# Optimization experiments

Measured on AMD Instinct MI355X. Metric: run time of the kernel, lower is better.

## Reference

```python
import jax, jax.numpy as jnp
import numpy as np

N_NODES = 100000
N_EDGES = 3200000
C, H, F = 512, 256, 64


def spmm(edge_row, edge_col, edge_val, Z):
    # (A @ Z)[i] = sum over edges e with row[e]==i of val[e] * Z[col[e]]
    msgs = edge_val[:, None] * Z[edge_col]  # [E, d]
    return jax.ops.segment_sum(msgs, edge_row, num_segments=N_NODES)


def setup_inputs() -> dict:
    key = jax.random.key(0)
    k1, k2, k3, k4, k5, k6, k7 = jax.random.split(key, 7)
    X = jax.random.normal(k1, (N_NODES, C), dtype=jnp.float32)
    edge_row = jax.random.randint(k2, (N_EDGES,), 0, N_NODES, dtype=jnp.int32)
    edge_col = jax.random.randint(k3, (N_EDGES,), 0, N_NODES, dtype=jnp.int32)
    edge_val = jax.random.uniform(k4, (N_EDGES,), dtype=jnp.float32)
    W0 = jax.random.normal(k5, (C, H), dtype=jnp.float32) * (C ** -0.5)
    Wh1 = jax.random.normal(k6, (H, H), dtype=jnp.float32) * (H ** -0.5)
    W1 = jax.random.normal(k7, (H, F), dtype=jnp.float32) * (H ** -0.5)
    return {"X": X, "edge_row": edge_row, "edge_col": edge_col,
            "edge_val": edge_val, "W0": W0, "Wh1": Wh1, "W1": W1}


def reference(X, edge_row, edge_col, edge_val, W0, Wh1, W1):
    # layer 0: relu(A @ (X W0))   (dropout=0 -> identity)
    Z = jax.nn.relu(spmm(edge_row, edge_col, edge_val, X @ W0))
    # hidden layers (num_layers - 2 = 1)
    Z = jax.nn.relu(spmm(edge_row, edge_col, edge_val, Z @ Wh1))
    # output layer: softmax(A @ (Z W1), axis=-1)
    Z = jax.nn.softmax(spmm(edge_row, edge_col, edge_val, Z @ W1), axis=-1)
    return Z
```

## Files before the change

kernel.cpp:

```cpp
#include <hip/hip_runtime.h>
#include <cstdint>
#include <cstddef>


#define SCAN_B 1024

typedef __attribute__((ext_vector_type(8))) short short8_t;
typedef __attribute__((ext_vector_type(4))) short short4_t;
typedef __attribute__((ext_vector_type(4))) float f32x4;

__device__ __forceinline__ short bf16_hi(float x) {
    union { float f; unsigned u; } c; c.f = x;
    return (short)(c.u >> 16);
}
__device__ __forceinline__ float bf16_f32(short h) {
    union { float f; unsigned u; } c; c.u = ((unsigned)(unsigned short)h) << 16;
    return c.f;
}

__device__ __forceinline__ void gload_lds16(const void* g, void* l) {
    __builtin_amdgcn_global_load_lds(
        (const __attribute__((address_space(1))) void*)g,
        (__attribute__((address_space(3))) void*)l, 16, 0, 0);
}


__global__ void count_rows_k(const int* __restrict__ row, int* __restrict__ deg, int E) {
    int e = blockIdx.x * blockDim.x + threadIdx.x;
    if (e < E) atomicAdd(&deg[row[e]], 1);
}

__global__ __launch_bounds__(SCAN_B) void scan1_k(const int* __restrict__ deg,
                                                  int* __restrict__ part,
                                                  int* __restrict__ bsum, int n) {
    __shared__ int buf[SCAN_B];
    int tid = threadIdx.x;
    int i = blockIdx.x * SCAN_B + tid;
    int v = (i < n) ? ((deg[i] + 3) & ~3) : 0;
    buf[tid] = v;
    __syncthreads();
    for (int off = 1; off < SCAN_B; off <<= 1) {
        int y = (tid >= off) ? buf[tid - off] : 0;
        __syncthreads();
        buf[tid] += y;
        __syncthreads();
    }
    if (i < n) part[i] = buf[tid] - v;
    if (tid == SCAN_B - 1) bsum[blockIdx.x] = buf[tid];
}

__global__ __launch_bounds__(128) void scan2_k(int* __restrict__ bsum, int nb) {
    __shared__ int buf[128];
    int tid = threadIdx.x;
    int v = (tid < nb) ? bsum[tid] : 0;
    buf[tid] = v;
    __syncthreads();
    for (int off = 1; off < 128; off <<= 1) {
        int y = (tid >= off) ? buf[tid - off] : 0;
        __syncthreads();
        buf[tid] += y;
        __syncthreads();
    }
    if (tid < nb) bsum[tid] = buf[tid] - v;
    if (tid == nb - 1) bsum[nb] = buf[tid];
}

__global__ __launch_bounds__(SCAN_B) void scan3_k(int* __restrict__ rowptr,
                                                  const int* __restrict__ bsum,
                                                  int* __restrict__ cursor, int n, int nb) {
    int i = blockIdx.x * SCAN_B + threadIdx.x;
    if (i < n) {
        int v = rowptr[i] + bsum[blockIdx.x];
        rowptr[i] = v;
        cursor[i] = v;
    }
    if (i == 0) rowptr[n] = bsum[nb];
}

__global__ void scatter_k(const int* __restrict__ row, const int* __restrict__ col,
                          const float* __restrict__ val, int* __restrict__ cursor,
                          int2* __restrict__ ecv, int E) {
    int e = blockIdx.x * blockDim.x + threadIdx.x;
    if (e < E) {
        int r = row[e];
        int p = atomicAdd(&cursor[r], 1);
        ecv[p] = make_int2(col[e], __float_as_int(val[e]));
    }
}


__global__ void split_w_k(const float* __restrict__ W, short* __restrict__ Bhl,
                          int K, int M) {
    int i = blockIdx.x * 256 + threadIdx.x;
    if (i >= K * M) return;
    int k = i / M, m = i - k * M;
    float x = W[i];
    short hi = bf16_hi(x);
    float r = x - bf16_f32(hi);
    short lo = bf16_hi(r);
    int g = k >> 3, j = k & 7;
    Bhl[(size_t)m * (2 * K) + 16 * g + j] = hi;
    Bhl[(size_t)m * (2 * K) + 16 * g + 8 + j] = lo;
}


template <int K, int BN, int NWR, int NWC, bool AF32>
__global__ __launch_bounds__(256) void gemm_hl(const void* __restrict__ Av,
                                               const short* __restrict__ Bhl,
                                               short* __restrict__ ZQ,
                                               float* __restrict__ scl, int N) {
    constexpr int BM = 64 * NWR;
    constexpr int NF = BN / NWC / 16;
    constexpr int NT = K / 32;
    __shared__ short Ald[2][BM * 64];
    __shared__ short Bld[2][BN * 64];

    const int tid = threadIdx.x, lane = tid & 63, w = tid >> 6;
    const int wr = w / NWC, wc = w % NWC;
    const int row0 = blockIdx.x * BM;
    const int l8 = lane >> 3;
    const int sx = (lane & 7) ^ l8;

    const short* Ahl = (const short*)Av;
    const float* Af  = (const float*)Av;
    const int arow = tid >> 2, aq = tid & 3;
    const int akey = arow & 7;

    f32x4 acc[4][NF] = {};

    auto stageB = [&](int t, int b) {
#pragma unroll
        for (int ch = w; ch < BN / 8; ch += 4)
            gload_lds16(Bhl + (size_t)(ch * 8 + l8) * (2 * K) + (size_t)t * 64 + sx * 8,
                        &Bld[b][ch * 512]);
    };
    auto stageAg = [&](int t, int b) {
#pragma unroll
        for (int ch = w; ch < BM / 8; ch += 4)
            gload_lds16(Ahl + (size_t)(row0 + ch * 8 + l8) * (2 * K) + (size_t)t * 64 + sx * 8,
                        &Ald[b][ch * 512]);
    };
    auto loadAf = [&](int t, float4& x0, float4& x1) {
        int gr = row0 + arow;
        x0 = make_float4(0.f, 0.f, 0.f, 0.f); x1 = x0;
        if (gr < N) {
            x0 = *(const float4*)&Af[(size_t)gr * K + t * 32 + aq * 8];
            x1 = *(const float4*)&Af[(size_t)gr * K + t * 32 + aq * 8 + 4];
        }
    };
    auto writeAf = [&](int b, float4 x0, float4 x1) {
        float f[8] = {x0.x, x0.y, x0.z, x0.w, x1.x, x1.y, x1.z, x1.w};
        short8_t hi, lo;
#pragma unroll
        for (int j = 0; j < 8; ++j) {
            short hh = bf16_hi(f[j]);
            hi[j] = hh;
            lo[j] = bf16_hi(f[j] - bf16_f32(hh));
        }
        *(short8_t*)&Ald[b][arow * 64 + ((2 * aq) ^ akey) * 8] = hi;
        *(short8_t*)&Ald[b][arow * 64 + ((2 * aq + 1) ^ akey) * 8] = lo;
    };

    if constexpr (AF32) {
        float4 x0, x1;
        loadAf(0, x0, x1);
        writeAf(0, x0, x1);
    } else {
        stageAg(0, 0);
    }
    stageB(0, 0);
    __syncthreads();

    for (int t = 0; t < NT; ++t) {
        const int cur = t & 1, nxt = cur ^ 1;
        float4 px0, px1;
        if (t + 1 < NT) {
            if constexpr (AF32) loadAf(t + 1, px0, px1);
            else                stageAg(t + 1, nxt);
            stageB(t + 1, nxt);
        }

        const int sH = (lane >> 4) * 2, sL = sH + 1;
        short8_t ah[4], al[4];
#pragma unroll
        for (int m = 0; m < 4; ++m) {
            int rl = wr * 64 + m * 16 + (lane & 15);
            int key = rl & 7;
            ah[m] = *(const short8_t*)&Ald[cur][rl * 64 + (sH ^ key) * 8];
            al[m] = *(const short8_t*)&Ald[cur][rl * 64 + (sL ^ key) * 8];
        }
#pragma unroll
        for (int n = 0; n < NF; ++n) {
            int cl = wc * (BN / NWC) + n * 16 + (lane & 15);
            int key = cl & 7;
            short8_t bh = *(const short8_t*)&Bld[cur][cl * 64 + (sH ^ key) * 8];
            short8_t bl = *(const short8_t*)&Bld[cur][cl * 64 + (sL ^ key) * 8];
#pragma unroll
            for (int m = 0; m < 4; ++m) {
                acc[m][n] = __builtin_amdgcn_mfma_f32_16x16x32_bf16(ah[m], bh, acc[m][n], 0, 0, 0);
                acc[m][n] = __builtin_amdgcn_mfma_f32_16x16x32_bf16(ah[m], bl, acc[m][n], 0, 0, 0);
                acc[m][n] = __builtin_amdgcn_mfma_f32_16x16x32_bf16(al[m], bh, acc[m][n], 0, 0, 0);
            }
        }
        if constexpr (AF32) {
            if (t + 1 < NT) writeAf(nxt, px0, px1);
        }
        __syncthreads();
    }

    const int lg = lane >> 4, lc = lane & 15;
    float* maxb = (float*)&Ald[0][0];
    float rmax[4][4];
#pragma unroll
    for (int m = 0; m < 4; ++m)
#pragma unroll
        for (int r = 0; r < 4; ++r) {
            float v = 0.f;
#pragma unroll
            for (int n = 0; n < NF; ++n) v = fmaxf(v, fabsf(acc[m][n][r]));
#pragma unroll
            for (int o = 8; o >= 1; o >>= 1) v = fmaxf(v, __shfl_xor(v, o));
            rmax[m][r] = v;
        }
    if constexpr (NWC > 1) {
        if (lc == 0)
#pragma unroll
            for (int m = 0; m < 4; ++m)
#pragma unroll
                for (int r = 0; r < 4; ++r)
                    maxb[(wr * 64 + m * 16 + lg * 4 + r) * NWC + wc] = rmax[m][r];
        __syncthreads();
    }
#pragma unroll
    for (int m = 0; m < 4; ++m)
#pragma unroll
        for (int r = 0; r < 4; ++r) {
            int rl = wr * 64 + m * 16 + lg * 4 + r;
            float v = rmax[m][r];
            if constexpr (NWC > 1) {
                v = maxb[rl * NWC];
#pragma unroll
                for (int q = 1; q < NWC; ++q) v = fmaxf(v, maxb[rl * NWC + q]);
            }
            int grow = row0 + rl;
            if (grow < N) {
                float inv = (v > 0.f) ? 32767.f / v : 0.f;
                if (lc == 0 && wc == 0) scl[grow] = v * (1.f / 32767.f);
#pragma unroll
                for (int n = 0; n < NF; ++n)
                    ZQ[(size_t)grow * BN + wc * (BN / NWC) + n * 16 + lc] =
                        (short)rintf(acc[m][n][r] * inv);
            }
        }
}


__global__ __launch_bounds__(256) void spmm_agg256_k(const int* __restrict__ rowptr,
                                                     const int2* __restrict__ ecv,
                                                     const short* __restrict__ Q,
                                                     const float* __restrict__ scl,
                                                     short* __restrict__ Zhl, int N) {
    int row = blockIdx.x * 4 + (threadIdx.x >> 6);
    if (row >= N) return;
    int lane = threadIdx.x & 63;
    int s = rowptr[row], e = rowptr[row + 1];
    const short4_t* Qv = (const short4_t*)Q;
    f32x4 acc = {0.f, 0.f, 0.f, 0.f};
    for (int i = s; i < e; i += 4) {
        int4 a = *(const int4*)(ecv + i);
        int4 b = *(const int4*)(ecv + i + 2);
        float w0 = __int_as_float(a.y) * scl[a.x];
        float w1 = __int_as_float(a.w) * scl[a.z];
        float w2 = __int_as_float(b.y) * scl[b.x];
        float w3 = __int_as_float(b.w) * scl[b.z];
        short4_t q0 = Qv[(size_t)a.x * 64 + lane];
        short4_t q1 = Qv[(size_t)a.z * 64 + lane];
        short4_t q2 = Qv[(size_t)b.x * 64 + lane];
        short4_t q3 = Qv[(size_t)b.z * 64 + lane];
#pragma unroll
        for (int j = 0; j < 4; ++j) {
            acc[j] = fmaf(w0, (float)q0[j], acc[j]);
            acc[j] = fmaf(w1, (float)q1[j], acc[j]);
            acc[j] = fmaf(w2, (float)q2[j], acc[j]);
            acc[j] = fmaf(w3, (float)q3[j], acc[j]);
        }
    }
    short4_t hi, lo;
#pragma unroll
    for (int j = 0; j < 4; ++j) {
        float r = fmaxf(acc[j], 0.f);
        short h = bf16_hi(r);
        hi[j] = h;
        lo[j] = bf16_hi(r - bf16_f32(h));
    }
    size_t base = (size_t)row * 512 + (lane >> 1) * 16 + (lane & 1) * 4;
    *(short4_t*)&Zhl[base] = hi;
    *(short4_t*)&Zhl[base + 8] = lo;
}

__global__ __launch_bounds__(256) void spmm_softmax64_k(const int* __restrict__ rowptr,
                                                        const int2* __restrict__ ecv,
                                                        const short* __restrict__ Q,
                                                        const float* __restrict__ scl,
                                                        float* __restrict__ out, int N) {
    int row = blockIdx.x * 4 + (threadIdx.x >> 6);
    if (row >= N) return;
    int lane = threadIdx.x & 63;
    int s = rowptr[row], e = rowptr[row + 1];
    float acc = 0.f;
    for (int i = s; i < e; i += 4) {
        int4 a = *(const int4*)(ecv + i);
        int4 b = *(const int4*)(ecv + i + 2);
        float w0 = __int_as_float(a.y) * scl[a.x];
        float w1 = __int_as_float(a.w) * scl[a.z];
        float w2 = __int_as_float(b.y) * scl[b.x];
        float w3 = __int_as_float(b.w) * scl[b.z];
        float z0 = (float)Q[(size_t)a.x * 64 + lane];
        float z1 = (float)Q[(size_t)a.z * 64 + lane];
        float z2 = (float)Q[(size_t)b.x * 64 + lane];
        float z3 = (float)Q[(size_t)b.z * 64 + lane];
        acc = fmaf(w0, z0, acc);
        acc = fmaf(w1, z1, acc);
        acc = fmaf(w2, z2, acc);
        acc = fmaf(w3, z3, acc);
    }
    float m = acc;
#pragma unroll
    for (int o = 32; o >= 1; o >>= 1) m = fmaxf(m, __shfl_xor(m, o));
    float p = __expf(acc - m);
    float ssum = p;
#pragma unroll
    for (int o = 32; o >= 1; o >>= 1) ssum += __shfl_xor(ssum, o);
    out[(size_t)row * 64 + lane] = p / ssum;
}


extern "C" void kernel_launch(void* const* d_in, const int* in_sizes, int n_in,
                              void* d_out, int out_size, void* d_ws, size_t ws_size,
                              hipStream_t stream) {
    const float* X        = (const float*)d_in[0];
    const int*   edge_row = (const int*)d_in[1];
    const int*   edge_col = (const int*)d_in[2];
    const float* edge_val = (const float*)d_in[3];
    const float* W0       = (const float*)d_in[4];
    const float* Wh1      = (const float*)d_in[5];
    const float* W1       = (const float*)d_in[6];

    const int C = 512, H = 256, F = 64;
    const int N = in_sizes[0] / C;
    const int E = in_sizes[1];
    const int EPAD = E + 4 * N + 64;

    size_t off = 0;
    auto alloc = [&](size_t bytes) -> void* {
        void* p = (char*)d_ws + off;
        off += (bytes + 255) & ~(size_t)255;
        return p;
    };
    short* Zhl    = (short*)alloc((size_t)N * 2 * H * sizeof(short));
    short* ZQ     = (short*)alloc((size_t)N * H * sizeof(short));
    float* scl    = (float*)alloc((size_t)N * sizeof(float));
    int*   deg    = (int*)alloc((size_t)N * sizeof(int));
    int*   rowptr = (int*)alloc((size_t)(N + 1) * sizeof(int));
    int*   cursor = (int*)alloc((size_t)N * sizeof(int));
    int*   bsum   = (int*)alloc(129 * sizeof(int));
    int2*  ecv    = (int2*)alloc((size_t)EPAD * sizeof(int2));
    short* Bhl0   = (short*)alloc((size_t)H * 2 * C * sizeof(short));
    short* Bhl1   = (short*)alloc((size_t)H * 2 * H * sizeof(short));
    short* Bhl2   = (short*)alloc((size_t)F * 2 * H * sizeof(short));
    (void)ws_size;

    hipMemsetAsync(deg, 0, (size_t)N * sizeof(int), stream);
    hipMemsetAsync(ecv, 0, (size_t)EPAD * sizeof(int2), stream);
    count_rows_k<<<(E + 255) / 256, 256, 0, stream>>>(edge_row, deg, E);
    int nb = (N + SCAN_B - 1) / SCAN_B;
    scan1_k<<<nb, SCAN_B, 0, stream>>>(deg, rowptr, bsum, N);
    scan2_k<<<1, 128, 0, stream>>>(bsum, nb);
    scan3_k<<<nb, SCAN_B, 0, stream>>>(rowptr, bsum, cursor, N, nb);
    scatter_k<<<(E + 255) / 256, 256, 0, stream>>>(edge_row, edge_col, edge_val,
                                                   cursor, ecv, E);

    split_w_k<<<(C * H + 255) / 256, 256, 0, stream>>>(W0, Bhl0, C, H);
    split_w_k<<<(H * H + 255) / 256, 256, 0, stream>>>(Wh1, Bhl1, H, H);
    split_w_k<<<(H * F + 255) / 256, 256, 0, stream>>>(W1, Bhl2, H, F);

    const int g64  = (N + 63) / 64;
    const int g128 = (N + 127) / 128;
    const int rg   = (N + 3) / 4;

    gemm_hl<512, 256, 1, 4, true><<<g64, 256, 0, stream>>>(X, Bhl0, ZQ, scl, N);
    spmm_agg256_k<<<rg, 256, 0, stream>>>(rowptr, ecv, ZQ, scl, Zhl, N);
    gemm_hl<256, 256, 1, 4, false><<<g64, 256, 0, stream>>>(Zhl, Bhl1, ZQ, scl, N);
    spmm_agg256_k<<<rg, 256, 0, stream>>>(rowptr, ecv, ZQ, scl, Zhl, N);
    gemm_hl<256, 64, 2, 2, false><<<g128, 256, 0, stream>>>(Zhl, Bhl2, ZQ, scl, N);
    spmm_softmax64_k<<<rg, 256, 0, stream>>>(rowptr, ecv, ZQ, scl,
                                             (float*)d_out, N);
}
```

Measured before the change: 1.168 ms.

## Partition CSR scatter by XCD and split edges across half-waves in SpMM

```diff
diff --git a/kernel.cpp b/kernel.cpp
--- a/kernel.cpp
+++ b/kernel.cpp
@@ -77,14 +77,22 @@
     if (i == 0) rowptr[n] = bsum[nb];
 }
 
-__global__ void scatter_k(const int* __restrict__ row, const int* __restrict__ col,
-                          const float* __restrict__ val, int* __restrict__ cursor,
-                          int2* __restrict__ ecv, int E) {
-    int e = blockIdx.x * blockDim.x + threadIdx.x;
-    if (e < E) {
+__global__ __launch_bounds__(256) void scatter_xcd_k(const int* __restrict__ row,
+                                                     const int* __restrict__ col,
+                                                     const float* __restrict__ val,
+                                                     int* __restrict__ cursor,
+                                                     int2* __restrict__ ecv,
+                                                     int E, int gsz) {
+    const int g = blockIdx.x & 7;
+    const int rank = blockIdx.x >> 3;
+    const int R = gridDim.x >> 3;
+    const int lo = g * gsz, hi = lo + gsz;
+    for (int e = rank * 256 + threadIdx.x; e < E; e += R * 256) {
         int r = row[e];
-        int p = atomicAdd(&cursor[r], 1);
-        ecv[p] = make_int2(col[e], __float_as_int(val[e]));
+        if (r >= lo && r < hi) {
+            int p = atomicAdd(&cursor[r], 1);
+            ecv[p] = make_int2(col[e], __float_as_int(val[e]));
+        }
     }
 }
 
@@ -262,40 +270,48 @@
                                                      short* __restrict__ Zhl, int N) {
     int row = blockIdx.x * 4 + (threadIdx.x >> 6);
     if (row >= N) return;
-    int lane = threadIdx.x & 63;
+    const int lane = threadIdx.x & 63;
+    const int half = lane >> 5;
+    const int l32 = lane & 31;
     int s = rowptr[row], e = rowptr[row + 1];
-    const short4_t* Qv = (const short4_t*)Q;
-    f32x4 acc = {0.f, 0.f, 0.f, 0.f};
+    const short8_t* Qv = (const short8_t*)Q;
+    f32x4 a0 = {0.f, 0.f, 0.f, 0.f}, a1 = a0;
     for (int i = s; i < e; i += 4) {
-        int4 a = *(const int4*)(ecv + i);
-        int4 b = *(const int4*)(ecv + i + 2);
-        float w0 = __int_as_float(a.y) * scl[a.x];
-        float w1 = __int_as_float(a.w) * scl[a.z];
-        float w2 = __int_as_float(b.y) * scl[b.x];
-        float w3 = __int_as_float(b.w) * scl[b.z];
-        short4_t q0 = Qv[(size_t)a.x * 64 + lane];
-        short4_t q1 = Qv[(size_t)a.z * 64 + lane];
-        short4_t q2 = Qv[(size_t)b.x * 64 + lane];
-        short4_t q3 = Qv[(size_t)b.z * 64 + lane];
+        int4 A = *(const int4*)(ecv + i);
+        int4 B = *(const int4*)(ecv + i + 2);
+        int   cA = half ? A.z : A.x;
+        float wA = __int_as_float(half ? A.w : A.y) * scl[cA];
+        int   cB = half ? B.z : B.x;
+        float wB = __int_as_float(half ? B.w : B.y) * scl[cB];
+        short8_t qA = Qv[(size_t)cA * 32 + l32];
+        short8_t qB = Qv[(size_t)cB * 32 + l32];
 #pragma unroll
         for (int j = 0; j < 4; ++j) {
-            acc[j] = fmaf(w0, (float)q0[j], acc[j]);
-            acc[j] = fmaf(w1, (float)q1[j], acc[j]);
-            acc[j] = fmaf(w2, (float)q2[j], acc[j]);
-            acc[j] = fmaf(w3, (float)q3[j], acc[j]);
-        }
-    }
-    short4_t hi, lo;
+            a0[j] = fmaf(wA, (float)qA[j], a0[j]);
+            a1[j] = fmaf(wA, (float)qA[j + 4], a1[j]);
+            a0[j] = fmaf(wB, (float)qB[j], a0[j]);
+            a1[j] = fmaf(wB, (float)qB[j + 4], a1[j]);
+        }
+    }
 #pragma unroll
     for (int j = 0; j < 4; ++j) {
-        float r = fmaxf(acc[j], 0.f);
-        short h = bf16_hi(r);
-        hi[j] = h;
-        lo[j] = bf16_hi(r - bf16_f32(h));
-    }
-    size_t base = (size_t)row * 512 + (lane >> 1) * 16 + (lane & 1) * 4;
-    *(short4_t*)&Zhl[base] = hi;
-    *(short4_t*)&Zhl[base + 8] = lo;
+        a0[j] += __shfl_xor(a0[j], 32);
+        a1[j] += __shfl_xor(a1[j], 32);
+    }
+    if (half == 0) {
+        short8_t hi, lo;
+#pragma unroll
+        for (int j = 0; j < 4; ++j) {
+            float r0 = fmaxf(a0[j], 0.f), r1 = fmaxf(a1[j], 0.f);
+            short h0 = bf16_hi(r0), h1 = bf16_hi(r1);
+            hi[j] = h0; hi[j + 4] = h1;
+            lo[j] = bf16_hi(r0 - bf16_f32(h0));
+            lo[j + 4] = bf16_hi(r1 - bf16_f32(h1));
+        }
+        size_t base = (size_t)row * 512 + l32 * 16;
+        *(short8_t*)&Zhl[base] = hi;
+        *(short8_t*)&Zhl[base + 8] = lo;
+    }
 }
 
 __global__ __launch_bounds__(256) void spmm_softmax64_k(const int* __restrict__ rowptr,
@@ -305,33 +321,40 @@
                                                         float* __restrict__ out, int N) {
     int row = blockIdx.x * 4 + (threadIdx.x >> 6);
     if (row >= N) return;
-    int lane = threadIdx.x & 63;
+    const int lane = threadIdx.x & 63;
+    const int q = lane >> 4;
+    const int l16 = lane & 15;
     int s = rowptr[row], e = rowptr[row + 1];
-    float acc = 0.f;
+    const short4_t* Qv = (const short4_t*)Q;
+    f32x4 acc = {0.f, 0.f, 0.f, 0.f};
     for (int i = s; i < e; i += 4) {
-        int4 a = *(const int4*)(ecv + i);
-        int4 b = *(const int4*)(ecv + i + 2);
-        float w0 = __int_as_float(a.y) * scl[a.x];
-        float w1 = __int_as_float(a.w) * scl[a.z];
-        float w2 = __int_as_float(b.y) * scl[b.x];
-        float w3 = __int_as_float(b.w) * scl[b.z];
-        float z0 = (float)Q[(size_t)a.x * 64 + lane];
-        float z1 = (float)Q[(size_t)a.z * 64 + lane];
-        float z2 = (float)Q[(size_t)b.x * 64 + lane];
-        float z3 = (float)Q[(size_t)b.z * 64 + lane];
-        acc = fmaf(w0, z0, acc);
-        acc = fmaf(w1, z1, acc);
-        acc = fmaf(w2, z2, acc);
-        acc = fmaf(w3, z3, acc);
-    }
-    float m = acc;
-#pragma unroll
-    for (int o = 32; o >= 1; o >>= 1) m = fmaxf(m, __shfl_xor(m, o));
-    float p = __expf(acc - m);
-    float ssum = p;
-#pragma unroll
-    for (int o = 32; o >= 1; o >>= 1) ssum += __shfl_xor(ssum, o);
-    out[(size_t)row * 64 + lane] = p / ssum;
+        int4 A = *(const int4*)(ecv + i);
+        int4 B = *(const int4*)(ecv + i + 2);
+        int c = (q & 2) ? ((q & 1) ? B.z : B.x) : ((q & 1) ? A.z : A.x);
+        int wbits = (q & 2) ? ((q & 1) ? B.w : B.y) : ((q & 1) ? A.w : A.y);
+        float wv = __int_as_float(wbits) * scl[c];
+        short4_t z = Qv[(size_t)c * 16 + l16];
+#pragma unroll
+        for (int j = 0; j < 4; ++j) acc[j] = fmaf(wv, (float)z[j], acc[j]);
+    }
+#pragma unroll
+    for (int j = 0; j < 4; ++j) {
+        acc[j] += __shfl_xor(acc[j], 16);
+        acc[j] += __shfl_xor(acc[j], 32);
+    }
+    float m = fmaxf(fmaxf(acc[0], acc[1]), fmaxf(acc[2], acc[3]));
+#pragma unroll
+    for (int o = 8; o >= 1; o >>= 1) m = fmaxf(m, __shfl_xor(m, o));
+    float p0 = __expf(acc[0] - m), p1 = __expf(acc[1] - m);
+    float p2 = __expf(acc[2] - m), p3 = __expf(acc[3] - m);
+    float ssum = p0 + p1 + p2 + p3;
+#pragma unroll
+    for (int o = 8; o >= 1; o >>= 1) ssum += __shfl_xor(ssum, o);
+    if (q == 0) {
+        float inv = 1.f / ssum;
+        float4 o4 = make_float4(p0 * inv, p1 * inv, p2 * inv, p3 * inv);
+        *(float4*)&out[(size_t)row * 64 + l16 * 4] = o4;
+    }
 }
 
 
@@ -377,8 +400,9 @@
     scan1_k<<<nb, SCAN_B, 0, stream>>>(deg, rowptr, bsum, N);
     scan2_k<<<1, 128, 0, stream>>>(bsum, nb);
     scan3_k<<<nb, SCAN_B, 0, stream>>>(rowptr, bsum, cursor, N, nb);
-    scatter_k<<<(E + 255) / 256, 256, 0, stream>>>(edge_row, edge_col, edge_val,
-                                                   cursor, ecv, E);
+    const int gsz = (N + 7) / 8;
+    scatter_xcd_k<<<8 * 256, 256, 0, stream>>>(edge_row, edge_col, edge_val,
+                                               cursor, ecv, E, gsz);
 
     split_w_k<<<(C * H + 255) / 256, 256, 0, stream>>>(W0, Bhl0, C, H);
     split_w_k<<<(H * H + 255) / 256, 256, 0, stream>>>(Wh1, Bhl1, H, H);
```

Result: faster. 1.124 ms (-3.8%).
